# Kernel tuning notes

Hardware: AMD Instinct MI355X
Metric: run time of the kernel (lower is better)

Reference implementation:

```python
import jax, jax.numpy as jnp
import numpy as np

N_NODES = 20000
N_EDGES = 640000
C_IN = 128      # num_node_features
K_FOLDS = 8     # num_edge_features
FILTERS = 128


def setup_inputs() -> dict:
    key = jax.random.key(0)
    k1, k2, k3, k4, k5, k6 = jax.random.split(key, 6)
    node_features = jax.random.normal(k1, (N_NODES, C_IN), dtype=jnp.float32)
    edge_features = jax.random.uniform(k2, (K_FOLDS, N_EDGES), dtype=jnp.float32)
    rows = jax.random.randint(k3, (N_EDGES,), 0, N_NODES)
    cols = jax.random.randint(k4, (N_EDGES,), 0, N_NODES)
    indices = jnp.stack([rows, cols], axis=1).astype(jnp.int64)
    # glorot_uniform kernel [K, C_in, filters]
    limit = np.sqrt(6.0 / (C_IN + FILTERS))
    kernel = jax.random.uniform(k5, (K_FOLDS, C_IN, FILTERS), dtype=jnp.float32,
                                minval=-limit, maxval=limit)
    bias = jnp.zeros((FILTERS,), dtype=jnp.float32)
    return {
        "node_features": node_features,
        "edge_features": edge_features,
        "kernel": kernel,
        "bias": bias,
        "indices": indices,
        "out_size": N_NODES,
    }


def reference(node_features, edge_features, kernel, bias, indices, out_size):
    # fold_conv: out[i,f] = sum_{e: row(e)=i} sum_k ef[k,e] * (x[col(e)] @ kernel[k])[f]
    row = indices[:, 0]
    col = indices[:, 1]
    xg = node_features[col]  # [E, C] gathered source-node features
    E = xg.shape[0]
    msgs = jnp.zeros((E, kernel.shape[2]), dtype=node_features.dtype)
    # Loop over the small fixed number of folds (K=8); each iteration is a
    # dense [E,C]x[C,F] matmul scaled by the per-edge fold weight.
    for k in range(kernel.shape[0]):
        msgs = msgs + (xg @ kernel[k]) * edge_features[k][:, None]
    out = jax.ops.segment_sum(msgs, row, num_segments=out_size)  # [out_size, F]
    out = out + bias  # bias_add; activation is None (linear)
    return out
```

## Files before the change

kernel.cpp:

```cpp
#include <hip/hip_runtime.h>
#include <cstddef>
#include <cstdint>

static constexpr int kNodes   = 20000;
static constexpr int kEdges   = 640000;
static constexpr int kCin     = 128;
static constexpr int kFolds   = 8;
static constexpr int kFilters = 128;
static constexpr int kKdim    = kFolds * kCin;
static constexpr int kCap     = 80;

typedef __attribute__((ext_vector_type(8))) short v8s;
typedef __attribute__((ext_vector_type(4))) float v4f;

__device__ __forceinline__ unsigned short f2bf(float f) {
    union { float f; uint32_t u; } v; v.f = f;
    const uint32_t u = v.u;
    return (unsigned short)((u + 0x7fffu + ((u >> 16) & 1u)) >> 16);
}
__device__ __forceinline__ float bf2f(unsigned short s) {
    union { uint32_t u; float f; } v; v.u = ((uint32_t)s) << 16;
    return v.f;
}

__global__ __launch_bounds__(256) void prep_k(
    const int2*  __restrict__ idx2,
    const float* __restrict__ ef,
    const float* __restrict__ x,
    const float* __restrict__ W,
    int* __restrict__ cnt,
    int* __restrict__ ebuf,
    unsigned int* __restrict__ rec,
    unsigned short* __restrict__ xb,
    unsigned short* __restrict__ Wt)
{
    const int b = blockIdx.x;
    const int t = threadIdx.x;
    if (b < 2500) {
        const int e = b * 256 + t;
        const int2 rc = idx2[e];
        union { uint4 q; unsigned int w[4]; unsigned short s[8]; } o;
        #pragma unroll
        for (int k = 0; k < kFolds; ++k)
            o.s[k] = f2bf(ef[(size_t)k * kEdges + e]);
        uint4* recp = (uint4*)(rec + (size_t)e * 8);
        recp[0] = make_uint4((unsigned)rc.y, o.w[0], o.w[1], o.w[2]);
        recp[1] = make_uint4(o.w[3], 0u, 0u, 0u);
        const int p = atomicAdd(&cnt[rc.x], 1);
        if (p < kCap) ebuf[rc.x * kCap + p] = e;
    } else if (b < 3750) {
        const int i = (b - 2500) * 2048 + t * 8;
        const float4 a = *(const float4*)(x + i);
        const float4 c = *(const float4*)(x + i + 4);
        union { uint4 q; unsigned short s[8]; } o;
        o.s[0] = f2bf(a.x); o.s[1] = f2bf(a.y); o.s[2] = f2bf(a.z); o.s[3] = f2bf(a.w);
        o.s[4] = f2bf(c.x); o.s[5] = f2bf(c.y); o.s[6] = f2bf(c.z); o.s[7] = f2bf(c.w);
        *(uint4*)(xb + i) = o.q;
    } else {
        const int t2 = (b - 3750) * 256 + t;
        const int n  = t2 & 127;
        const int k8 = t2 >> 7;
        union { uint4 q; unsigned short s[8]; } o;
        #pragma unroll
        for (int j = 0; j < 8; ++j)
            o.s[j] = f2bf(W[(size_t)(k8 * 8 + j) * kFilters + n]);
        *(uint4*)(Wt + (size_t)n * kKdim + k8 * 8) = o.q;
    }
}

__global__ __launch_bounds__(64) void pull_k(
    const unsigned short* __restrict__ xb,
    const int*  __restrict__ ebuf,
    const unsigned int* __restrict__ rec,
    const int*  __restrict__ cnt,
    unsigned short* __restrict__ S)
{
    __shared__ int   sCol[4][kCap];
    __shared__ float sEf[4][kCap][8];
    __shared__ int   sDeg[4];

    const int t  = threadIdx.x;
    const int n0 = blockIdx.x * 4;

    if (t < 4) {
        int d = cnt[n0 + t];
        sDeg[t] = d < kCap ? d : kCap;
    }
    #pragma unroll
    for (int gg = 0; gg < 4; ++gg) {
        const int nn = n0 + gg;
        int dg = cnt[nn];
        dg = dg < kCap ? dg : kCap;
        for (int s = t; s < dg; s += 64) {
            const int e = ebuf[nn * kCap + s];
            const uint4 q0   = *(const uint4*)(rec + (size_t)e * 8);
            const unsigned w3 = rec[(size_t)e * 8 + 4];
            sCol[gg][s] = (int)q0.x;
            sEf[gg][s][0] = bf2f((unsigned short)(q0.y));
            sEf[gg][s][1] = bf2f((unsigned short)(q0.y >> 16));
            sEf[gg][s][2] = bf2f((unsigned short)(q0.z));
            sEf[gg][s][3] = bf2f((unsigned short)(q0.z >> 16));
            sEf[gg][s][4] = bf2f((unsigned short)(q0.w));
            sEf[gg][s][5] = bf2f((unsigned short)(q0.w >> 16));
            sEf[gg][s][6] = bf2f((unsigned short)(w3));
            sEf[gg][s][7] = bf2f((unsigned short)(w3 >> 16));
        }
    }
    __syncthreads();

    const int g  = t >> 4;
    const int c8 = (t & 15) * 8;
    const int n  = n0 + g;
    const int deg = sDeg[g];

    float acc[8][8];
    #pragma unroll
    for (int k = 0; k < 8; ++k)
        #pragma unroll
        for (int j = 0; j < 8; ++j) acc[k][j] = 0.f;

    const unsigned short* xbase = xb + c8;
    v8s xcur;
    if (deg > 0) xcur = *(const v8s*)(xbase + (size_t)sCol[g][0] * kCin);

    for (int i = 0; i < deg; ++i) {
        const int nidx = (i + 1 < deg) ? i + 1 : i;
        const v8s xnext = *(const v8s*)(xbase + (size_t)sCol[g][nidx] * kCin);

        float xf[8];
        #pragma unroll
        for (int j = 0; j < 8; ++j) xf[j] = bf2f((unsigned short)xcur[j]);

        const float4 wa = *(const float4*)&sEf[g][i][0];
        const float4 wc = *(const float4*)&sEf[g][i][4];
        const float w[8] = {wa.x, wa.y, wa.z, wa.w, wc.x, wc.y, wc.z, wc.w};

        #pragma unroll
        for (int k = 0; k < 8; ++k)
            #pragma unroll
            for (int j = 0; j < 8; ++j)
                acc[k][j] += w[k] * xf[j];

        xcur = xnext;
    }

    unsigned short* srow = S + (size_t)n * kKdim + c8;
    #pragma unroll
    for (int k = 0; k < 8; ++k) {
        union { uint4 q; unsigned short s[8]; } o;
        #pragma unroll
        for (int j = 0; j < 8; ++j) o.s[j] = f2bf(acc[k][j]);
        *(uint4*)(srow + k * kCin) = o.q;
    }
}

static constexpr int BM  = 64;
static constexpr int BK  = 32;
static constexpr int SWS = 40;

__global__ __launch_bounds__(256) void gemm_k(
    const unsigned short* __restrict__ S,
    const unsigned short* __restrict__ Wt,
    const float* __restrict__ bias,
    float* __restrict__ out)
{
    __shared__ unsigned short sS[BM * SWS];
    __shared__ unsigned short sWt[kFilters * SWS];

    const int t    = threadIdx.x;
    const int wave = t >> 6;
    const int lane = t & 63;
    const int quad = lane >> 4;
    const int r16  = lane & 15;
    const int m0   = blockIdx.x * BM;

    v4f acc[8];
    #pragma unroll
    for (int i = 0; i < 8; ++i) acc[i] = (v4f){0.f, 0.f, 0.f, 0.f};

    for (int k0 = 0; k0 < kKdim; k0 += BK) {
        {
            const int row = t >> 2;
            const int kc  = (t & 3) * 8;
            const int m   = m0 + row;
            uint4 v = make_uint4(0, 0, 0, 0);
            if (m < kNodes)
                v = *(const uint4*)(S + (size_t)m * kKdim + k0 + kc);
            *(uint4*)&sS[row * SWS + kc] = v;
        }
        {
            const int n    = t >> 1;
            const int half = (t & 1) * 16;
            const unsigned short* src = Wt + (size_t)n * kKdim + k0 + half;
            *(uint4*)&sWt[n * SWS + half]     = *(const uint4*)(src);
            *(uint4*)&sWt[n * SWS + half + 8] = *(const uint4*)(src + 8);
        }
        __syncthreads();

        const v8s a = *(const v8s*)&sS[(wave * 16 + r16) * SWS + quad * 8];
        #pragma unroll
        for (int nt = 0; nt < 8; ++nt) {
            const v8s b = *(const v8s*)&sWt[(nt * 16 + r16) * SWS + quad * 8];
            acc[nt] = __builtin_amdgcn_mfma_f32_16x16x32_bf16(a, b, acc[nt], 0, 0, 0);
        }
        __syncthreads();
    }

    #pragma unroll
    for (int nt = 0; nt < 8; ++nt) {
        const int n = nt * 16 + r16;
        const float bv = bias[n];
        #pragma unroll
        for (int r = 0; r < 4; ++r) {
            const int m = m0 + wave * 16 + quad * 4 + r;
            if (m < kNodes)
                out[(size_t)m * kFilters + n] = acc[nt][r] + bv;
        }
    }
}

extern "C" void kernel_launch(void* const* d_in, const int* in_sizes, int n_in,
                              void* d_out, int out_size, void* d_ws, size_t ws_size,
                              hipStream_t stream) {
    const float* x    = (const float*)d_in[0];
    const float* ef   = (const float*)d_in[1];
    const float* W    = (const float*)d_in[2];
    const float* bias = (const float*)d_in[3];
    const int2*  idx2 = (const int2*)d_in[4];
    float* out = (float*)d_out;

    char* ws = (char*)d_ws;
    unsigned short* S    = (unsigned short*)(ws);
    unsigned int*   rec  = (unsigned int*)(ws + 40960000);
    int*            ebuf = (int*)(ws + 61440000);
    unsigned short* xb   = (unsigned short*)(ws + 67840000);
    unsigned short* Wt   = (unsigned short*)(ws + 72960000);
    int*            cnt  = (int*)(ws + 73222144);

    hipMemsetAsync(cnt, 0, kNodes * sizeof(int), stream);

    prep_k<<<3814, 256, 0, stream>>>(idx2, ef, x, W, cnt, ebuf, rec, xb, Wt);
    pull_k<<<kNodes / 4, 64, 0, stream>>>(xb, ebuf, rec, cnt, S);
    gemm_k<<<(kNodes + BM - 1) / BM, 256, 0, stream>>>(S, Wt, bias, out);
}
```

Measured before the change: 190.7 us.

## Replace global per-row atomic binning with two-pass bucketed edge binning

Building the per-row edge lists used to take one global atomicAdd per edge on the row counters. It now runs in two passes. First, extra blocks in the prep kernel build shared-memory histograms over 250 buckets of 80 rows, reserve space with one global atomic per bucket, and scatter (row, edge) pairs. Then a new bin2 kernel uses shared-memory atomics to build the per-row lists and write the counts. This is meant to cut global atomic contention and scattered writes, at the cost of an extra kernel launch and an intermediate pairs buffer that reuses the S workspace region.

After: 185.4 us. 2.8% less time.

```diff
diff --git a/kernel.cpp b/kernel.cpp
--- a/kernel.cpp
+++ b/kernel.cpp
@@ -10,6 +10,11 @@
 static constexpr int kKdim    = kFolds * kCin;
 static constexpr int kCap     = 80;
 
+static constexpr int kNBucket = 250;
+static constexpr int kRowsPB  = 80;
+static constexpr int kCapB    = 3072;
+static constexpr int kBin1Blk = 160;
+
 typedef __attribute__((ext_vector_type(8))) short v8s;
 typedef __attribute__((ext_vector_type(4))) float v4f;
 
@@ -28,8 +33,8 @@
     const float* __restrict__ ef,
     const float* __restrict__ x,
     const float* __restrict__ W,
-    int* __restrict__ cnt,
-    int* __restrict__ ebuf,
+    int* __restrict__ bucketCnt,
+    int2* __restrict__ pairs,
     unsigned int* __restrict__ rec,
     unsigned short* __restrict__ xb,
     unsigned short* __restrict__ Wt)
@@ -46,8 +51,6 @@
         uint4* recp = (uint4*)(rec + (size_t)e * 8);
         recp[0] = make_uint4((unsigned)rc.y, o.w[0], o.w[1], o.w[2]);
         recp[1] = make_uint4(o.w[3], 0u, 0u, 0u);
-        const int p = atomicAdd(&cnt[rc.x], 1);
-        if (p < kCap) ebuf[rc.x * kCap + p] = e;
     } else if (b < 3750) {
         const int i = (b - 2500) * 2048 + t * 8;
         const float4 a = *(const float4*)(x + i);
@@ -56,7 +59,7 @@
         o.s[0] = f2bf(a.x); o.s[1] = f2bf(a.y); o.s[2] = f2bf(a.z); o.s[3] = f2bf(a.w);
         o.s[4] = f2bf(c.x); o.s[5] = f2bf(c.y); o.s[6] = f2bf(c.z); o.s[7] = f2bf(c.w);
         *(uint4*)(xb + i) = o.q;
-    } else {
+    } else if (b < 3814) {
         const int t2 = (b - 3750) * 256 + t;
         const int n  = t2 & 127;
         const int k8 = t2 >> 7;
@@ -65,7 +68,75 @@
         for (int j = 0; j < 8; ++j)
             o.s[j] = f2bf(W[(size_t)(k8 * 8 + j) * kFilters + n]);
         *(uint4*)(Wt + (size_t)n * kKdim + k8 * 8) = o.q;
-    }
+    } else {
+        __shared__ int hist[kNBucket];
+        __shared__ int base[kNBucket];
+        const int bb = b - 3814;
+        const int e0 = bb * 4096;
+
+        if (t < kNBucket) hist[t] = 0;
+        __syncthreads();
+
+        int rowsReg[16];
+        #pragma unroll
+        for (int i = 0; i < 16; ++i) {
+            const int e = e0 + i * 256 + t;
+            int row = -1;
+            if (e < kEdges) {
+                row = idx2[e].x;
+                atomicAdd(&hist[row / kRowsPB], 1);
+            }
+            rowsReg[i] = row;
+        }
+        __syncthreads();
+
+        if (t < kNBucket) {
+            const int h = hist[t];
+            base[t] = atomicAdd(&bucketCnt[t], h);
+            hist[t] = 0;
+        }
+        __syncthreads();
+
+        #pragma unroll
+        for (int i = 0; i < 16; ++i) {
+            const int row = rowsReg[i];
+            if (row >= 0) {
+                const int e  = e0 + i * 256 + t;
+                const int bk = row / kRowsPB;
+                const int sl = base[bk] + atomicAdd(&hist[bk], 1);
+                if (sl < kCapB)
+                    pairs[(size_t)bk * kCapB + sl] = make_int2(row, e);
+            }
+        }
+    }
+}
+
+__global__ __launch_bounds__(256) void bin2_k(
+    const int2* __restrict__ pairs,
+    const int*  __restrict__ bucketCnt,
+    int* __restrict__ ebuf,
+    int* __restrict__ cnt)
+{
+    __shared__ int c80[kRowsPB];
+    const int b = blockIdx.x;
+    const int t = threadIdx.x;
+
+    if (t < kRowsPB) c80[t] = 0;
+    __syncthreads();
+
+    int n = bucketCnt[b];
+    n = n < kCapB ? n : kCapB;
+    const int2* seg = pairs + (size_t)b * kCapB;
+
+    for (int s = t; s < n; s += 256) {
+        const int2 p = seg[s];
+        const int rl = p.x - b * kRowsPB;
+        const int c  = atomicAdd(&c80[rl], 1);
+        if (c < kCap) ebuf[p.x * kCap + c] = p.y;
+    }
+    __syncthreads();
+
+    if (t < kRowsPB) cnt[b * kRowsPB + t] = c80[t];
 }
 
 __global__ __launch_bounds__(64) void pull_k(
@@ -230,16 +301,20 @@
     float* out = (float*)d_out;
 
     char* ws = (char*)d_ws;
-    unsigned short* S    = (unsigned short*)(ws);
-    unsigned int*   rec  = (unsigned int*)(ws + 40960000);
-    int*            ebuf = (int*)(ws + 61440000);
-    unsigned short* xb   = (unsigned short*)(ws + 67840000);
-    unsigned short* Wt   = (unsigned short*)(ws + 72960000);
-    int*            cnt  = (int*)(ws + 73222144);
-
-    hipMemsetAsync(cnt, 0, kNodes * sizeof(int), stream);
-
-    prep_k<<<3814, 256, 0, stream>>>(idx2, ef, x, W, cnt, ebuf, rec, xb, Wt);
+    unsigned short* S      = (unsigned short*)(ws);
+    int2*           pairs  = (int2*)(ws);
+    unsigned int*   rec    = (unsigned int*)(ws + 40960000);
+    int*            ebuf   = (int*)(ws + 61440000);
+    unsigned short* xb     = (unsigned short*)(ws + 67840000);
+    unsigned short* Wt     = (unsigned short*)(ws + 72960000);
+    int*            cnt    = (int*)(ws + 73222144);
+    int*            bucketCnt = (int*)(ws + 73302144);
+
+    hipMemsetAsync(bucketCnt, 0, kNBucket * sizeof(int), stream);
+
+    prep_k<<<3814 + kBin1Blk, 256, 0, stream>>>(idx2, ef, x, W, bucketCnt,
+                                                pairs, rec, xb, Wt);
+    bin2_k<<<kNBucket, 256, 0, stream>>>(pairs, bucketCnt, ebuf, cnt);
     pull_k<<<kNodes / 4, 64, 0, stream>>>(xb, ebuf, rec, cnt, S);
     gemm_k<<<(kNodes + BM - 1) / BM, 256, 0, stream>>>(S, Wt, bias, out);
 }
```
